# Kernel optimization log

Measured on AMD Instinct MI355X. Metric: run time of the kernel, lower is better.

## Reference

```python
import jax, jax.numpy as jnp
import numpy as np

N = 50000      # nodes
E = 800000     # edges (avg degree 16)
IN = 512       # input features
OUT = 32       # per-head hidden features
H = 8          # heads (layer 1)
C = 16         # classes (layer 2, 1 head)
NEG_SLOPE = 0.2


def setup_inputs() -> dict:
    key = jax.random.key(0)
    ks = jax.random.split(key, 8)
    x = jax.random.normal(ks[0], (N, IN), jnp.float32)
    edge_index = jax.random.randint(ks[1], (2, E), 0, N, jnp.int32)
    # layer 1 params: W1 [IN, H*OUT], attention vectors a1_src/a1_dst [H, OUT]
    W1 = jax.random.normal(ks[2], (IN, H * OUT), jnp.float32) * (1.0 / np.sqrt(IN))
    a1_src = jax.random.normal(ks[3], (H, OUT), jnp.float32) * (1.0 / np.sqrt(OUT))
    a1_dst = jax.random.normal(ks[4], (H, OUT), jnp.float32) * (1.0 / np.sqrt(OUT))
    # layer 2 params: single head, W2 [H*OUT, C], a2_src/a2_dst [1, C]
    W2 = jax.random.normal(ks[5], (H * OUT, C), jnp.float32) * (1.0 / np.sqrt(H * OUT))
    a2_src = jax.random.normal(ks[6], (1, C), jnp.float32) * (1.0 / np.sqrt(C))
    a2_dst = jax.random.normal(ks[7], (1, C), jnp.float32) * (1.0 / np.sqrt(C))
    return {"x": x, "W1": W1, "a1_src": a1_src, "a1_dst": a1_dst,
            "W2": W2, "a2_src": a2_src, "a2_dst": a2_dst,
            "edge_index": edge_index}


def gat_layer(x, edge_index, W, a_src, a_dst, concat):
    """Standard GAT layer: e_ij = LeakyReLU(a_src.Wh_i + a_dst.Wh_j),
    softmax over incoming edges of each target node, scatter-aggregate."""
    n = x.shape[0]
    h_heads, f = a_src.shape
    h = (x @ W).reshape(n, h_heads, f)                      # [N, H, F]
    src, dst = edge_index[0], edge_index[1]
    es = jnp.einsum('nhf,hf->nh', h, a_src)                 # [N, H] per-node src scores
    ed = jnp.einsum('nhf,hf->nh', h, a_dst)                 # [N, H]
    e = jax.nn.leaky_relu(es[src] + ed[dst], NEG_SLOPE)     # [E, H] per-edge logits
    # segment softmax over edges grouped by dst node
    m = jax.ops.segment_max(e, dst, num_segments=n)         # [N, H]
    m = jnp.where(jnp.isfinite(m), m, 0.0)                  # empty segments -> -inf
    p = jnp.exp(e - m[dst])                                 # [E, H]
    s = jax.ops.segment_sum(p, dst, num_segments=n)         # [N, H]
    denom = s[dst]
    alpha = p / jnp.where(denom > 0, denom, 1.0)            # [E, H]
    msg = h[src] * alpha[:, :, None]                        # [E, H, F]
    out = jax.ops.segment_sum(msg, dst, num_segments=n)     # [N, H, F]
    if concat:
        return out.reshape(n, h_heads * f)
    return out.mean(axis=1)


def reference(x, W1, a1_src, a1_dst, W2, a2_src, a2_dst, edge_index):
    # dropout is identity in eval mode
    h = gat_layer(x, edge_index, W1, a1_src, a1_dst, concat=True)   # [N, H*OUT]
    h = jax.nn.elu(h)
    h = gat_layer(h, edge_index, W2, a2_src, a2_dst, concat=False)  # [N, C]
    return jax.nn.log_softmax(h, axis=1)
```

## Files before the change

### kernel.cpp

```cpp
#include <hip/hip_runtime.h>

#define NN 50000
#define EE 800000
#define KIN 512
#define HF 256
#define NH 8
#define FOUT 32
#define NC 16
#define NEG 0.2f
#define NB_SCAN 196

typedef unsigned short u16;
typedef __attribute__((ext_vector_type(8))) short shortx8;
typedef __attribute__((ext_vector_type(4))) float floatx4;
typedef __attribute__((ext_vector_type(8))) unsigned short ushortx8;
typedef __attribute__((ext_vector_type(4))) unsigned uintx4;

__device__ __forceinline__ float lrelu(float x) { return x > 0.f ? x : NEG * x; }

__device__ __forceinline__ u16 f2bf(float f) {
    unsigned u = __float_as_uint(f);
    return (u16)((u + 0x7FFFu + ((u >> 16) & 1u)) >> 16);
}
__device__ __forceinline__ float bf2f(u16 v) {
    return __uint_as_float((unsigned)v << 16);
}
__device__ __forceinline__ unsigned pk2bf(float a, float b) {
    unsigned ua = __float_as_uint(a), ub = __float_as_uint(b);
    return ((ua + 0x8000u) >> 16) | ((ub + 0x8000u) & 0xffff0000u);
}

__device__ __forceinline__ void gll16(const void* g, void* l) {
    __builtin_amdgcn_global_load_lds((const __attribute__((address_space(1))) void*)g,
                                     (__attribute__((address_space(3))) void*)l, 16, 0, 0);
}

__global__ void count_deg_convw(const int* __restrict__ dst, int* __restrict__ deg,
                                const float* __restrict__ W1, const float* __restrict__ W2,
                                u16* __restrict__ w1t, u16* __restrict__ w2t) {
    int e = blockIdx.x * 256 + threadIdx.x;
    if (e < EE) atomicAdd(&deg[dst[e]], 1);
    if (e < KIN * HF) {
        int k = e >> 8, n = e & 255;
        w1t[n * KIN + k] = f2bf(W1[e]);
    } else if (e < KIN * HF + HF * NC) {
        int e2 = e - KIN * HF;
        int k = e2 >> 4, c = e2 & 15;
        w2t[c * HF + k] = f2bf(W2[e2]);
    }
}

__global__ __launch_bounds__(256) void scan_a(const int* __restrict__ deg, int* __restrict__ bsum) {
    __shared__ int sm[256];
    int t = threadIdx.x;
    int i = blockIdx.x * 256 + t;
    sm[t] = (i < NN) ? deg[i] : 0;
    __syncthreads();
    for (int o = 128; o; o >>= 1) { if (t < o) sm[t] += sm[t + o]; __syncthreads(); }
    if (t == 0) bsum[blockIdx.x] = sm[0];
}

__global__ __launch_bounds__(256) void scan_c(const int* __restrict__ deg, const int* __restrict__ bsum,
                                              int* __restrict__ off) {
    __shared__ int sm[256];
    __shared__ int pre[256];
    int t = threadIdx.x;
    pre[t] = (t < blockIdx.x && t < NB_SCAN) ? bsum[t] : 0;
    __syncthreads();
    for (int o = 128; o; o >>= 1) { if (t < o) pre[t] += pre[t + o]; __syncthreads(); }
    int bofs = pre[0];
    __syncthreads();
    int i = blockIdx.x * 256 + t;
    int d = (i < NN) ? deg[i] : 0;
    sm[t] = d;
    __syncthreads();
    for (int dd = 1; dd < 256; dd <<= 1) {
        int v = (t >= dd) ? sm[t - dd] : 0;
        __syncthreads();
        sm[t] += v;
        __syncthreads();
    }
    if (i < NN) off[i] = bofs + sm[t] - d;
    if (i == 0) off[NN] = EE;
}

__global__ void fill_csr(const int* __restrict__ src, const int* __restrict__ dst,
                         const int* __restrict__ off, int* __restrict__ cursor,
                         int* __restrict__ csr_src) {
    int e = blockIdx.x * 256 + threadIdx.x;
    if (e < EE) {
        int d = dst[e];
        int pos = atomicAdd(&cursor[d], 1);
        csr_src[off[d] + pos] = src[e];
    }
}

__global__ __launch_bounds__(256, 2) void gemm1_mfma(const float* __restrict__ x,
                                                     const u16* __restrict__ w1t,
                                                     u16* __restrict__ h1b,
                                                     const float* __restrict__ a1s,
                                                     const float* __restrict__ a1d,
                                                     float* __restrict__ es1,
                                                     float* __restrict__ ed1) {
    __shared__ __align__(16) float As[128 * 32];
    __shared__ __align__(16) u16 Bs[256 * 32];
    int t = threadIdx.x;
    int lane = t & 63, wave = t >> 6;
    int wm = wave >> 1, wn = wave & 1;
    int lm = lane & 15, quad = lane >> 4;
    int bm = blockIdx.x * 128;

    floatx4 acc[4][8];
#pragma unroll
    for (int i = 0; i < 4; i++)
#pragma unroll
        for (int j = 0; j < 8; j++) acc[i][j] = (floatx4){0.f, 0.f, 0.f, 0.f};

    int arow_l = wave * 32 + (lane >> 3);
    int akoff = (lane & 7) * 4;
    const float* aptr[4];
#pragma unroll
    for (int i = 0; i < 4; i++) {
        int ar = bm + arow_l + i * 8;
        if (ar > NN - 1) ar = NN - 1;
        aptr[i] = x + (size_t)ar * KIN + akoff;
    }
    float* alds[4];
#pragma unroll
    for (int i = 0; i < 4; i++) alds[i] = As + (wave * 32 + i * 8) * 32;

    int brow_l = wave * 64 + (lane >> 2);
    int bkoff = (lane & 3) * 8;
    const u16* bptr[4];
#pragma unroll
    for (int i = 0; i < 4; i++) bptr[i] = w1t + (size_t)(brow_l + i * 16) * KIN + bkoff;
    u16* blds[4];
#pragma unroll
    for (int i = 0; i < 4; i++) blds[i] = Bs + (wave * 64 + i * 16) * 32;

    int offA[4], offB[8];
#pragma unroll
    for (int i = 0; i < 4; i++) offA[i] = (wm * 64 + i * 16 + lm) * 32 + quad * 8;
#pragma unroll
    for (int j = 0; j < 8; j++) offB[j] = (wn * 128 + j * 16 + lm) * 32 + quad * 8;

    for (int kk = 0; kk < KIN; kk += 32) {
#pragma unroll
        for (int i = 0; i < 4; i++) gll16(aptr[i] + kk, alds[i]);
#pragma unroll
        for (int i = 0; i < 4; i++) gll16(bptr[i] + kk, blds[i]);
        __syncthreads();
        shortx8 af[4], bf[8];
#pragma unroll
        for (int i = 0; i < 4; i++) {
            const float4* ap = (const float4*)&As[offA[i]];
            float4 lo = ap[0], hi = ap[1];
            union { uintx4 u; shortx8 s; } cv;
            cv.u[0] = pk2bf(lo.x, lo.y);
            cv.u[1] = pk2bf(lo.z, lo.w);
            cv.u[2] = pk2bf(hi.x, hi.y);
            cv.u[3] = pk2bf(hi.z, hi.w);
            af[i] = cv.s;
        }
#pragma unroll
        for (int j = 0; j < 8; j++) bf[j] = *(const shortx8*)&Bs[offB[j]];
#pragma unroll
        for (int i = 0; i < 4; i++)
#pragma unroll
            for (int j = 0; j < 8; j++)
                acc[i][j] = __builtin_amdgcn_mfma_f32_16x16x32_bf16(af[i], bf[j], acc[i][j], 0, 0, 0);
        __syncthreads();
    }

#pragma unroll
    for (int i = 0; i < 4; i++) {
        int row = bm + wm * 64 + i * 16 + quad * 4;
#pragma unroll
        for (int j = 0; j < 8; j++) {
            int col = wn * 128 + j * 16 + lm;
#pragma unroll
            for (int r = 0; r < 4; r++) {
                if (row + r < NN) h1b[(size_t)(row + r) * HF + col] = f2bf(acc[i][j][r]);
            }
        }
    }

    float as_v[8], ad_v[8];
#pragma unroll
    for (int j = 0; j < 8; j++) {
        int col = wn * 128 + j * 16 + lm;
        as_v[j] = a1s[col];
        ad_v[j] = a1d[col];
    }
#pragma unroll
    for (int i = 0; i < 4; i++) {
#pragma unroll
        for (int r = 0; r < 4; r++) {
            int row = bm + wm * 64 + i * 16 + quad * 4 + r;
#pragma unroll
            for (int hp = 0; hp < 4; hp++) {
                float e_s = acc[i][2 * hp][r] * as_v[2 * hp] + acc[i][2 * hp + 1][r] * as_v[2 * hp + 1];
                float e_d = acc[i][2 * hp][r] * ad_v[2 * hp] + acc[i][2 * hp + 1][r] * ad_v[2 * hp + 1];
#pragma unroll
                for (int o = 8; o; o >>= 1) {
                    e_s += __shfl_down(e_s, o, 16);
                    e_d += __shfl_down(e_d, o, 16);
                }
                if (lm == 0 && row < NN) {
                    int h = wn * 4 + hp;
                    es1[row * NH + h] = e_s;
                    ed1[row * NH + h] = e_d;
                }
            }
        }
    }
}

__global__ __launch_bounds__(256) void agg1_mfma(const u16* __restrict__ h1b, const float* __restrict__ es,
                                                 const float* __restrict__ ed, const int* __restrict__ off,
                                                 const int* __restrict__ csr_src, u16* __restrict__ out1b) {
    __shared__ __align__(16) u16 Hs[32 * 256];
    __shared__ __align__(16) u16 pTs[8][32];
    __shared__ __align__(16) unsigned char dstloc[32];
    __shared__ int offs_s[17];
    __shared__ float ed_s[16][8];

    int t = threadIdx.x;
    int lane = t & 63, wave = t >> 6;
    int lm = lane & 15, quad = lane >> 4;
    int base = blockIdx.x * 16;

    if (t < 17) offs_s[t] = off[base + t];
    if (t < 128) ed_s[t >> 3][t & 7] = ed[(base + (t >> 3)) * NH + (t & 7)];
    int e0 = off[base];
    int e1 = off[base + 16];
    int nch = (e1 - e0 + 31) >> 5;
    __syncthreads();

    floatx4 acc[2][2];
    floatx4 accS[2];
#pragma unroll
    for (int a = 0; a < 2; a++) {
        accS[a] = (floatx4){0.f, 0.f, 0.f, 0.f};
#pragma unroll
        for (int b = 0; b < 2; b++) acc[a][b] = (floatx4){0.f, 0.f, 0.f, 0.f};
    }

    int h0 = 2 * wave;
    shortx8 ones;
#pragma unroll
    for (int i = 0; i < 8; i++) ones[i] = (short)0x3F80;

    int k_p = t >> 3, h_p = t & 7;
    int sv = 0;
    if (nch > 0) {
        int g = e0 + (lane & 31);
        sv = csr_src[g < e1 ? g : e1 - 1];
    }

    for (int c = 0; c < nch; c++) {
        int svn = 0;
        if (c + 1 < nch) {
            int g = e0 + ((c + 1) << 5) + (lane & 31);
            svn = csr_src[g < e1 ? g : e1 - 1];
        }
#pragma unroll
        for (int pass = 0; pass < 4; pass++) {
            int r = pass * 8 + 2 * wave + (lane >> 5);
            int s = __shfl(sv, r, 64);
            const u16* sp = h1b + (size_t)s * HF + (((lane & 31) ^ (pass << 1)) << 3);
            gll16(sp, Hs + pass * 2048 + wave * 512);
        }
        {
            int g = e0 + (c << 5) + k_p;
            int s = __shfl(sv, k_p, 64);
            float pv = 0.f;
            if (g < e1) {
                int m = 0;
                if (offs_s[m + 8] <= g) m += 8;
                if (offs_s[m + 4] <= g) m += 4;
                if (offs_s[m + 2] <= g) m += 2;
                if (offs_s[m + 1] <= g) m += 1;
                float lg = es[s * NH + h_p] + ed_s[m][h_p];
                lg = lg > 0.f ? lg : NEG * lg;
                pv = __expf(lg);
                if (h_p == 0) dstloc[k_p] = (unsigned char)m;
            }
            pTs[h_p][k_p] = f2bf(pv);
        }
        __syncthreads();

        union { uintx4 u; shortx8 s; } pa, pb, a0, a1;
        pa.s = *(const shortx8*)&pTs[h0][quad * 8];
        pb.s = *(const shortx8*)&pTs[h0 + 1][quad * 8];
        unsigned dw0 = *(const unsigned*)&dstloc[quad * 8];
        unsigned dw1 = *(const unsigned*)&dstloc[quad * 8 + 4];
        unsigned ulm = (unsigned)lm;
        unsigned mm0 = ((dw0 & 255u) == ulm ? 0xffffu : 0u) | (((dw0 >> 8) & 255u) == ulm ? 0xffff0000u : 0u);
        unsigned mm1 = (((dw0 >> 16) & 255u) == ulm ? 0xffffu : 0u) | ((dw0 >> 24) == ulm ? 0xffff0000u : 0u);
        unsigned mm2 = ((dw1 & 255u) == ulm ? 0xffffu : 0u) | (((dw1 >> 8) & 255u) == ulm ? 0xffff0000u : 0u);
        unsigned mm3 = (((dw1 >> 16) & 255u) == ulm ? 0xffffu : 0u) | ((dw1 >> 24) == ulm ? 0xffff0000u : 0u);
        a0.u[0] = pa.u[0] & mm0; a0.u[1] = pa.u[1] & mm1; a0.u[2] = pa.u[2] & mm2; a0.u[3] = pa.u[3] & mm3;
        a1.u[0] = pb.u[0] & mm0; a1.u[1] = pb.u[1] & mm1; a1.u[2] = pb.u[2] & mm2; a1.u[3] = pb.u[3] & mm3;

        accS[0] = __builtin_amdgcn_mfma_f32_16x16x32_bf16(a0.s, ones, accS[0], 0, 0, 0);
        accS[1] = __builtin_amdgcn_mfma_f32_16x16x32_bf16(a1.s, ones, accS[1], 0, 0, 0);

#pragma unroll
        for (int hh = 0; hh < 2; hh++) {
#pragma unroll
            for (int half = 0; half < 2; half++) {
                int f = (h0 + hh) * 32 + half * 16 + lm;
                int bidx = (quad * 8) * 256 + (((f >> 3) ^ (quad << 1)) << 3) + (f & 7);
                shortx8 bfv;
#pragma unroll
                for (int j = 0; j < 8; j++) bfv[j] = (short)Hs[bidx + j * 256];
                acc[hh][half] = __builtin_amdgcn_mfma_f32_16x16x32_bf16(
                    hh ? a1.s : a0.s, bfv, acc[hh][half], 0, 0, 0);
            }
        }
        __syncthreads();
        sv = svn;
    }

#pragma unroll
    for (int hh = 0; hh < 2; hh++) {
#pragma unroll
        for (int r = 0; r < 4; r++) {
            float sden = accS[hh][r];
            float inv = sden > 0.f ? 1.0f / sden : 0.f;
            int n = base + quad * 4 + r;
#pragma unroll
            for (int half = 0; half < 2; half++) {
                float v = acc[hh][half][r] * inv;
                v = v > 0.f ? v : (__expf(v) - 1.0f);
                out1b[(size_t)n * HF + (h0 + hh) * 32 + half * 16 + lm] = f2bf(v);
            }
        }
    }
}

__global__ __launch_bounds__(64) void gemm2_mfma(const u16* __restrict__ out1b, const u16* __restrict__ w2t,
                                                 const float* __restrict__ a2s, const float* __restrict__ a2d,
                                                 u16* __restrict__ h2b, float* __restrict__ es2,
                                                 float* __restrict__ ed2) {
    int lane = threadIdx.x;
    int lm = lane & 15, quad = lane >> 4;
    int nb = blockIdx.x * 16;
    floatx4 acc = (floatx4){0.f, 0.f, 0.f, 0.f};
    const u16* arow = out1b + (size_t)(nb + lm) * HF + quad * 8;
    const u16* brow = w2t + lm * HF + quad * 8;
#pragma unroll
    for (int kk = 0; kk < HF; kk += 32) {
        shortx8 af = *(const shortx8*)(arow + kk);
        shortx8 bf = *(const shortx8*)(brow + kk);
        acc = __builtin_amdgcn_mfma_f32_16x16x32_bf16(af, bf, acc, 0, 0, 0);
    }
    float a2sc = a2s[lm], a2dc = a2d[lm];
#pragma unroll
    for (int r = 0; r < 4; r++) {
        int n = nb + quad * 4 + r;
        float v = acc[r];
        h2b[n * NC + lm] = f2bf(v);
        float ps = v * a2sc, pd = v * a2dc;
#pragma unroll
        for (int o = 8; o; o >>= 1) {
            ps += __shfl_down(ps, o, 16);
            pd += __shfl_down(pd, o, 16);
        }
        if (lm == 0) { es2[n] = ps; ed2[n] = pd; }
    }
}

__global__ __launch_bounds__(256) void agg2(const u16* __restrict__ h2b, const float* __restrict__ es2,
                                            const float* __restrict__ ed2, const int* __restrict__ off,
                                            const int* __restrict__ csr_src, float* __restrict__ out) {
    int t = threadIdx.x;
    int nid = blockIdx.x * 16 + (t >> 4);
    int c = t & 15;
    int beg = off[nid];
    int deg = off[nid + 1] - beg;
    float edn = ed2[nid];
    float s = 0.f, acc = 0.f;
    for (int base = 0; base < deg; base += 16) {
        int nch = deg - base; if (nch > 16) nch = 16;
        int sv = 0;
        if (c < nch) sv = csr_src[beg + base + c];
        int sva[16];
#pragma unroll
        for (int e = 0; e < 16; e++) sva[e] = __shfl(sv, e, 16);
        float hva[16];
#pragma unroll
        for (int e = 0; e < 16; e++) hva[e] = bf2f(h2b[sva[e] * NC + c]);
        float p = 0.f;
        if (c < nch) p = __expf(lrelu(es2[sv] + edn));
        s += p;
        float pa[16];
#pragma unroll
        for (int e = 0; e < 16; e++) pa[e] = __shfl(p, e, 16);
#pragma unroll
        for (int e = 0; e < 16; e++) acc += pa[e] * hva[e];
    }
#pragma unroll
    for (int o = 8; o; o >>= 1) s += __shfl_down(s, o, 16);
    s = __shfl(s, 0, 16);
    float v = (s > 0.f) ? acc / s : 0.f;
    float m2 = v;
#pragma unroll
    for (int o = 8; o; o >>= 1) m2 = fmaxf(m2, __shfl_down(m2, o, 16));
    m2 = __shfl(m2, 0, 16);
    float se = __expf(v - m2);
#pragma unroll
    for (int o = 8; o; o >>= 1) se += __shfl_down(se, o, 16);
    se = __shfl(se, 0, 16);
    out[nid * NC + c] = v - m2 - __logf(se);
}

extern "C" void kernel_launch(void* const* d_in, const int* in_sizes, int n_in,
                              void* d_out, int out_size, void* d_ws, size_t ws_size,
                              hipStream_t stream) {
    const float* x   = (const float*)d_in[0];
    const float* W1  = (const float*)d_in[1];
    const float* a1s = (const float*)d_in[2];
    const float* a1d = (const float*)d_in[3];
    const float* W2  = (const float*)d_in[4];
    const float* a2s = (const float*)d_in[5];
    const float* a2d = (const float*)d_in[6];
    const int*   ei  = (const int*)d_in[7];
    const int* srcv = ei;
    const int* dstv = ei + EE;
    float* out = (float*)d_out;

    u16* h1b    = (u16*)d_ws;
    u16* out1b  = h1b + (size_t)NN * HF;
    float* es1  = (float*)(out1b + (size_t)NN * HF);
    float* ed1  = es1 + (size_t)NN * NH;
    u16* h2b    = (u16*)(ed1 + (size_t)NN * NH);
    float* es2v = (float*)(h2b + (size_t)NN * NC);
    float* ed2v = es2v + NN;
    int* deg    = (int*)(ed2v + NN);
    int* cursor = deg + NN;
    int* offs   = cursor + NN;
    int* csr    = offs + NN + 1;
    int* bsum   = csr + EE;
    u16* w1t    = (u16*)(bsum + 256);
    u16* w2t    = w1t + (size_t)HF * KIN;

    hipMemsetAsync(deg, 0, 2 * NN * sizeof(int), stream);
    count_deg_convw<<<(EE + 255) / 256, 256, 0, stream>>>(dstv, deg, W1, W2, w1t, w2t);
    scan_a<<<NB_SCAN, 256, 0, stream>>>(deg, bsum);
    scan_c<<<NB_SCAN, 256, 0, stream>>>(deg, bsum, offs);
    fill_csr<<<(EE + 255) / 256, 256, 0, stream>>>(srcv, dstv, offs, cursor, csr);
    gemm1_mfma<<<(NN + 127) / 128, 256, 0, stream>>>(x, w1t, h1b, a1s, a1d, es1, ed1);
    agg1_mfma<<<NN / 16, 256, 0, stream>>>(h1b, es1, ed1, offs, csr, out1b);
    gemm2_mfma<<<NN / 16, 64, 0, stream>>>(out1b, w2t, a2s, a2d, h2b, es2v, ed2v);
    agg2<<<NN / 16, 256, 0, stream>>>(h2b, es2v, ed2v, offs, csr, out);
}
```

Before: 360.3 us.

## Split gemm1 over N halves and load operands directly into registers with double buffering

The first-layer GEMM drops LDS staging and reads A (fp32 x) and B (bf16 W1^T) fragments straight from global memory into registers. Loads are double-buffered so the next K-slice is fetched while MFMAs run on the current one. The output is split into two 128-column halves, one per block, which doubles the grid and halves the accumulator count per thread. In exchange, each x row is read twice from global memory and fetched with uncoalesced per-lane strided accesses, and the barriers are gone.

```diff
diff --git a/kernel.cpp b/kernel.cpp
--- a/kernel.cpp
+++ b/kernel.cpp
@@ -102,82 +102,81 @@
                                                      const float* __restrict__ a1d,
                                                      float* __restrict__ es1,
                                                      float* __restrict__ ed1) {
-    __shared__ __align__(16) float As[128 * 32];
-    __shared__ __align__(16) u16 Bs[256 * 32];
     int t = threadIdx.x;
     int lane = t & 63, wave = t >> 6;
     int wm = wave >> 1, wn = wave & 1;
     int lm = lane & 15, quad = lane >> 4;
-    int bm = blockIdx.x * 128;
-
-    floatx4 acc[4][8];
+    int bid = blockIdx.x;
+    int bm = (bid >> 1) * 128;
+    int bn = (bid & 1) * 128;
+
+    floatx4 acc[4][4];
 #pragma unroll
     for (int i = 0; i < 4; i++)
 #pragma unroll
-        for (int j = 0; j < 8; j++) acc[i][j] = (floatx4){0.f, 0.f, 0.f, 0.f};
-
-    int arow_l = wave * 32 + (lane >> 3);
-    int akoff = (lane & 7) * 4;
-    const float* aptr[4];
+        for (int j = 0; j < 4; j++) acc[i][j] = (floatx4){0.f, 0.f, 0.f, 0.f};
+
+    const float* ap[4];
 #pragma unroll
     for (int i = 0; i < 4; i++) {
-        int ar = bm + arow_l + i * 8;
+        int ar = bm + wm * 64 + i * 16 + lm;
         if (ar > NN - 1) ar = NN - 1;
-        aptr[i] = x + (size_t)ar * KIN + akoff;
-    }
-    float* alds[4];
-#pragma unroll
-    for (int i = 0; i < 4; i++) alds[i] = As + (wave * 32 + i * 8) * 32;
-
-    int brow_l = wave * 64 + (lane >> 2);
-    int bkoff = (lane & 3) * 8;
-    const u16* bptr[4];
-#pragma unroll
-    for (int i = 0; i < 4; i++) bptr[i] = w1t + (size_t)(brow_l + i * 16) * KIN + bkoff;
-    u16* blds[4];
-#pragma unroll
-    for (int i = 0; i < 4; i++) blds[i] = Bs + (wave * 64 + i * 16) * 32;
-
-    int offA[4], offB[8];
-#pragma unroll
-    for (int i = 0; i < 4; i++) offA[i] = (wm * 64 + i * 16 + lm) * 32 + quad * 8;
-#pragma unroll
-    for (int j = 0; j < 8; j++) offB[j] = (wn * 128 + j * 16 + lm) * 32 + quad * 8;
-
-    for (int kk = 0; kk < KIN; kk += 32) {
-#pragma unroll
-        for (int i = 0; i < 4; i++) gll16(aptr[i] + kk, alds[i]);
-#pragma unroll
-        for (int i = 0; i < 4; i++) gll16(bptr[i] + kk, blds[i]);
-        __syncthreads();
-        shortx8 af[4], bf[8];
-#pragma unroll
-        for (int i = 0; i < 4; i++) {
-            const float4* ap = (const float4*)&As[offA[i]];
-            float4 lo = ap[0], hi = ap[1];
-            union { uintx4 u; shortx8 s; } cv;
-            cv.u[0] = pk2bf(lo.x, lo.y);
-            cv.u[1] = pk2bf(lo.z, lo.w);
-            cv.u[2] = pk2bf(hi.x, hi.y);
-            cv.u[3] = pk2bf(hi.z, hi.w);
-            af[i] = cv.s;
-        }
-#pragma unroll
-        for (int j = 0; j < 8; j++) bf[j] = *(const shortx8*)&Bs[offB[j]];
-#pragma unroll
-        for (int i = 0; i < 4; i++)
-#pragma unroll
-            for (int j = 0; j < 8; j++)
-                acc[i][j] = __builtin_amdgcn_mfma_f32_16x16x32_bf16(af[i], bf[j], acc[i][j], 0, 0, 0);
-        __syncthreads();
-    }
+        ap[i] = x + (size_t)ar * KIN + quad * 8;
+    }
+    const u16* bp[4];
+#pragma unroll
+    for (int j = 0; j < 4; j++) {
+        int col = bn + wn * 64 + j * 16 + lm;
+        bp[j] = w1t + (size_t)col * KIN + quad * 8;
+    }
+
+    float4 A0[4][2], A1[4][2];
+    shortx8 B0[4], B1[4];
+
+#define G1_LOAD(Ax, Bx, KK)                                              \
+    {                                                                    \
+        _Pragma("unroll") for (int i = 0; i < 4; i++) {                  \
+            Ax[i][0] = *(const float4*)(ap[i] + (KK));                   \
+            Ax[i][1] = *(const float4*)(ap[i] + (KK) + 4);               \
+        }                                                                \
+        _Pragma("unroll") for (int j = 0; j < 4; j++)                    \
+            Bx[j] = *(const shortx8*)(bp[j] + (KK));                     \
+    }
+
+#define G1_STEP(Ax, Bx)                                                  \
+    {                                                                    \
+        shortx8 af[4];                                                   \
+        _Pragma("unroll") for (int i = 0; i < 4; i++) {                  \
+            union { uintx4 u; shortx8 s; } cv;                           \
+            cv.u[0] = pk2bf(Ax[i][0].x, Ax[i][0].y);                     \
+            cv.u[1] = pk2bf(Ax[i][0].z, Ax[i][0].w);                     \
+            cv.u[2] = pk2bf(Ax[i][1].x, Ax[i][1].y);                     \
+            cv.u[3] = pk2bf(Ax[i][1].z, Ax[i][1].w);                     \
+            af[i] = cv.s;                                                \
+        }                                                                \
+        _Pragma("unroll") for (int i = 0; i < 4; i++)                    \
+            _Pragma("unroll") for (int j = 0; j < 4; j++)                \
+                acc[i][j] = __builtin_amdgcn_mfma_f32_16x16x32_bf16(     \
+                    af[i], Bx[j], acc[i][j], 0, 0, 0);                   \
+    }
+
+    G1_LOAD(A0, B0, 0);
+#pragma unroll
+    for (int it = 0; it < 8; it++) {
+        G1_LOAD(A1, B1, it * 64 + 32);
+        G1_STEP(A0, B0);
+        if (it < 7) G1_LOAD(A0, B0, it * 64 + 64);
+        G1_STEP(A1, B1);
+    }
+#undef G1_LOAD
+#undef G1_STEP
 
 #pragma unroll
     for (int i = 0; i < 4; i++) {
         int row = bm + wm * 64 + i * 16 + quad * 4;
 #pragma unroll
-        for (int j = 0; j < 8; j++) {
-            int col = wn * 128 + j * 16 + lm;
+        for (int j = 0; j < 4; j++) {
+            int col = bn + wn * 64 + j * 16 + lm;
 #pragma unroll
             for (int r = 0; r < 4; r++) {
                 if (row + r < NN) h1b[(size_t)(row + r) * HF + col] = f2bf(acc[i][j][r]);
@@ -185,10 +184,10 @@
         }
     }
 
-    float as_v[8], ad_v[8];
-#pragma unroll
-    for (int j = 0; j < 8; j++) {
-        int col = wn * 128 + j * 16 + lm;
+    float as_v[4], ad_v[4];
+#pragma unroll
+    for (int j = 0; j < 4; j++) {
+        int col = bn + wn * 64 + j * 16 + lm;
         as_v[j] = a1s[col];
         ad_v[j] = a1d[col];
     }
@@ -198,7 +197,7 @@
         for (int r = 0; r < 4; r++) {
             int row = bm + wm * 64 + i * 16 + quad * 4 + r;
 #pragma unroll
-            for (int hp = 0; hp < 4; hp++) {
+            for (int hp = 0; hp < 2; hp++) {
                 float e_s = acc[i][2 * hp][r] * as_v[2 * hp] + acc[i][2 * hp + 1][r] * as_v[2 * hp + 1];
                 float e_d = acc[i][2 * hp][r] * ad_v[2 * hp] + acc[i][2 * hp + 1][r] * ad_v[2 * hp + 1];
 #pragma unroll
@@ -207,7 +206,7 @@
                     e_d += __shfl_down(e_d, o, 16);
                 }
                 if (lm == 0 && row < NN) {
-                    int h = wn * 4 + hp;
+                    int h = (bn >> 5) + wn * 2 + hp;
                     es1[row * NH + h] = e_s;
                     ed1[row * NH + h] = e_d;
                 }
@@ -451,7 +450,7 @@
     scan_a<<<NB_SCAN, 256, 0, stream>>>(deg, bsum);
     scan_c<<<NB_SCAN, 256, 0, stream>>>(deg, bsum, offs);
     fill_csr<<<(EE + 255) / 256, 256, 0, stream>>>(srcv, dstv, offs, cursor, csr);
-    gemm1_mfma<<<(NN + 127) / 128, 256, 0, stream>>>(x, w1t, h1b, a1s, a1d, es1, ed1);
+    gemm1_mfma<<<((NN + 127) / 128) * 2, 256, 0, stream>>>(x, w1t, h1b, a1s, a1d, es1, ed1);
     agg1_mfma<<<NN / 16, 256, 0, stream>>>(h1b, es1, ed1, offs, csr, out1b);
     gemm2_mfma<<<NN / 16, 64, 0, stream>>>(out1b, w2t, a2s, a2d, h2b, es2v, ed2v);
     agg2<<<NN / 16, 256, 0, stream>>>(h2b, es2v, ed2v, offs, csr, out);
```

Measured after the change: 436.4 us. +21.1%, slower.

## Shrink gemm1 row tile to 64 and re-layout LDS staging for occupancy

Applied to the files above, without the earlier changes.

The first-layer GEMM now processes 64 rows per block instead of 128, halving the accumulator registers per wave and raising the launch-bounds occupancy target from 2 to 3 blocks per CU. The LDS staging is reorganised into k-group-major layouts, where each 16-byte direct-to-LDS load covers one row's 4-float or 8-bf16 chunk and fragments are read from contiguous slices. The goal is more blocks in flight to hide global-load latency and fewer LDS bank conflicts. In exchange, each W1 tile is reused across fewer rows, so total W1 traffic and the number of blocks both double.

```diff
diff --git a/kernel.cpp b/kernel.cpp
--- a/kernel.cpp
+++ b/kernel.cpp
@@ -95,66 +95,52 @@
     }
 }
 
-__global__ __launch_bounds__(256, 2) void gemm1_mfma(const float* __restrict__ x,
+__global__ __launch_bounds__(256, 3) void gemm1_mfma(const float* __restrict__ x,
                                                      const u16* __restrict__ w1t,
                                                      u16* __restrict__ h1b,
                                                      const float* __restrict__ a1s,
                                                      const float* __restrict__ a1d,
                                                      float* __restrict__ es1,
                                                      float* __restrict__ ed1) {
-    __shared__ __align__(16) float As[128 * 32];
-    __shared__ __align__(16) u16 Bs[256 * 32];
+    __shared__ __align__(16) float As[8 * 64 * 4];
+    __shared__ __align__(16) u16 Bs[4 * 256 * 8];
     int t = threadIdx.x;
     int lane = t & 63, wave = t >> 6;
     int wm = wave >> 1, wn = wave & 1;
     int lm = lane & 15, quad = lane >> 4;
-    int bm = blockIdx.x * 128;
-
-    floatx4 acc[4][8];
-#pragma unroll
-    for (int i = 0; i < 4; i++)
+    int bm = blockIdx.x * 64;
+
+    floatx4 acc[2][8];
+#pragma unroll
+    for (int i = 0; i < 2; i++)
 #pragma unroll
         for (int j = 0; j < 8; j++) acc[i][j] = (floatx4){0.f, 0.f, 0.f, 0.f};
 
-    int arow_l = wave * 32 + (lane >> 3);
-    int akoff = (lane & 7) * 4;
-    const float* aptr[4];
-#pragma unroll
-    for (int i = 0; i < 4; i++) {
-        int ar = bm + arow_l + i * 8;
-        if (ar > NN - 1) ar = NN - 1;
-        aptr[i] = x + (size_t)ar * KIN + akoff;
-    }
-    float* alds[4];
-#pragma unroll
-    for (int i = 0; i < 4; i++) alds[i] = As + (wave * 32 + i * 8) * 32;
-
-    int brow_l = wave * 64 + (lane >> 2);
-    int bkoff = (lane & 3) * 8;
-    const u16* bptr[4];
-#pragma unroll
-    for (int i = 0; i < 4; i++) bptr[i] = w1t + (size_t)(brow_l + i * 16) * KIN + bkoff;
-    u16* blds[4];
-#pragma unroll
-    for (int i = 0; i < 4; i++) blds[i] = Bs + (wave * 64 + i * 16) * 32;
-
-    int offA[4], offB[8];
-#pragma unroll
-    for (int i = 0; i < 4; i++) offA[i] = (wm * 64 + i * 16 + lm) * 32 + quad * 8;
-#pragma unroll
-    for (int j = 0; j < 8; j++) offB[j] = (wn * 128 + j * 16 + lm) * 32 + quad * 8;
+    int arow = bm + lane;
+    if (arow > NN - 1) arow = NN - 1;
+    const float* axp = x + (size_t)arow * KIN;
+    const u16* bxp[4];
+#pragma unroll
+    for (int b = 0; b < 4; b++) bxp[b] = w1t + (size_t)(b * 64 + lane) * KIN + wave * 8;
 
     for (int kk = 0; kk < KIN; kk += 32) {
 #pragma unroll
-        for (int i = 0; i < 4; i++) gll16(aptr[i] + kk, alds[i]);
-#pragma unroll
-        for (int i = 0; i < 4; i++) gll16(bptr[i] + kk, blds[i]);
-        __syncthreads();
-        shortx8 af[4], bf[8];
-#pragma unroll
-        for (int i = 0; i < 4; i++) {
-            const float4* ap = (const float4*)&As[offA[i]];
-            float4 lo = ap[0], hi = ap[1];
+        for (int a = 0; a < 2; a++) {
+            int g = wave * 2 + a;
+            gll16(axp + kk + g * 4, &As[g * 64 * 4]);
+        }
+#pragma unroll
+        for (int b = 0; b < 4; b++)
+            gll16(bxp[b] + kk, &Bs[(wave * 256 + b * 64) * 8]);
+        __syncthreads();
+
+        shortx8 af[2], bf[8];
+#pragma unroll
+        for (int i = 0; i < 2; i++) {
+            int row = wm * 32 + i * 16 + lm;
+            int g0 = quad * 2;
+            float4 lo = *(const float4*)&As[(g0 * 64 + row) * 4];
+            float4 hi = *(const float4*)&As[((g0 + 1) * 64 + row) * 4];
             union { uintx4 u; shortx8 s; } cv;
             cv.u[0] = pk2bf(lo.x, lo.y);
             cv.u[1] = pk2bf(lo.z, lo.w);
@@ -163,9 +149,12 @@
             af[i] = cv.s;
         }
 #pragma unroll
-        for (int j = 0; j < 8; j++) bf[j] = *(const shortx8*)&Bs[offB[j]];
-#pragma unroll
-        for (int i = 0; i < 4; i++)
+        for (int j = 0; j < 8; j++) {
+            int col = wn * 128 + j * 16 + lm;
+            bf[j] = *(const shortx8*)&Bs[(quad * 256 + col) * 8];
+        }
+#pragma unroll
+        for (int i = 0; i < 2; i++)
 #pragma unroll
             for (int j = 0; j < 8; j++)
                 acc[i][j] = __builtin_amdgcn_mfma_f32_16x16x32_bf16(af[i], bf[j], acc[i][j], 0, 0, 0);
@@ -173,8 +162,8 @@
     }
 
 #pragma unroll
-    for (int i = 0; i < 4; i++) {
-        int row = bm + wm * 64 + i * 16 + quad * 4;
+    for (int i = 0; i < 2; i++) {
+        int row = bm + wm * 32 + i * 16 + quad * 4;
 #pragma unroll
         for (int j = 0; j < 8; j++) {
             int col = wn * 128 + j * 16 + lm;
@@ -193,10 +182,10 @@
         ad_v[j] = a1d[col];
     }
 #pragma unroll
-    for (int i = 0; i < 4; i++) {
+    for (int i = 0; i < 2; i++) {
 #pragma unroll
         for (int r = 0; r < 4; r++) {
-            int row = bm + wm * 64 + i * 16 + quad * 4 + r;
+            int row = bm + wm * 32 + i * 16 + quad * 4 + r;
 #pragma unroll
             for (int hp = 0; hp < 4; hp++) {
                 float e_s = acc[i][2 * hp][r] * as_v[2 * hp] + acc[i][2 * hp + 1][r] * as_v[2 * hp + 1];
@@ -451,7 +440,7 @@
     scan_a<<<NB_SCAN, 256, 0, stream>>>(deg, bsum);
     scan_c<<<NB_SCAN, 256, 0, stream>>>(deg, bsum, offs);
     fill_csr<<<(EE + 255) / 256, 256, 0, stream>>>(srcv, dstv, offs, cursor, csr);
-    gemm1_mfma<<<(NN + 127) / 128, 256, 0, stream>>>(x, w1t, h1b, a1s, a1d, es1, ed1);
+    gemm1_mfma<<<(NN + 63) / 64, 256, 0, stream>>>(x, w1t, h1b, a1s, a1d, es1, ed1);
     agg1_mfma<<<NN / 16, 256, 0, stream>>>(h1b, es1, ed1, offs, csr, out1b);
     gemm2_mfma<<<NN / 16, 64, 0, stream>>>(out1b, w2t, a2s, a2d, h2b, es2v, ed2v);
     agg2<<<NN / 16, 256, 0, stream>>>(h2b, es2v, ed2v, offs, csr, out);
```

After: 394.1 us. +9.4%, slower.
